# Optimization experiments

Measured on AMD Instinct MI355X. Metric: run time of the kernel, lower is better.

## Reference

```python
import jax, jax.numpy as jnp
import numpy as np

B, T, N = 32, 2048, 2048
D, L, TE, H = 512, 256, 1024, 8

def _ln(x, g, b, eps=1e-5):
    m = x.mean(-1, keepdims=True)
    v = ((x - m) ** 2).mean(-1, keepdims=True)
    return (x - m) / jnp.sqrt(v + eps) * g + b

def setup_inputs() -> dict:
    key = jax.random.key(0)
    ks = jax.random.split(key, 12)
    s = 0.02
    return {
        "x": jax.random.normal(ks[0], (B, T, D), jnp.float32),
        "xf": jax.random.normal(ks[1], (B, N, L), jnp.float32),
        "emb": jax.random.normal(ks[2], (B, TE), jnp.float32),
        "norm_g": jnp.ones((D,), jnp.float32),
        "norm_b": jnp.zeros((D,), jnp.float32),
        "tnorm_g": jnp.ones((L,), jnp.float32),
        "tnorm_b": jnp.zeros((L,), jnp.float32),
        "Wq": jax.random.normal(ks[3], (D, D), jnp.float32) * s,
        "bq": jnp.zeros((D,), jnp.float32),
        "Wk": jax.random.normal(ks[4], (L, D), jnp.float32) * s,
        "bk": jnp.zeros((D,), jnp.float32),
        "Wv": jax.random.normal(ks[5], (L, D), jnp.float32) * s,
        "bv": jnp.zeros((D,), jnp.float32),
        "We": jax.random.normal(ks[6], (TE, 2 * D), jnp.float32) * s,
        "be": jnp.zeros((2 * D,), jnp.float32),
        "snorm_g": jnp.ones((D,), jnp.float32),
        "snorm_b": jnp.zeros((D,), jnp.float32),
        "Wo": jax.random.normal(ks[7], (D, D), jnp.float32) * s,
        "bo": jnp.zeros((D,), jnp.float32),
    }

def reference(x, xf, emb, norm_g, norm_b, tnorm_g, tnorm_b, Wq, bq, Wk, bk, Wv, bv,
              We, be, snorm_g, snorm_b, Wo, bo):
    b, t, d = x.shape
    n = xf.shape[1]
    hd = d // H
    # projections with pre-LayerNorms
    q = (_ln(x, norm_g, norm_b) @ Wq + bq).reshape(b, t, H, hd)
    xfn = _ln(xf, tnorm_g, tnorm_b)
    k = (xfn @ Wk + bk).reshape(b, n, H, hd)
    v = (xfn @ Wv + bv).reshape(b, n, H, hd)
    # dual softmax of linear attention: query over head-dim, key over sequence
    q = jax.nn.softmax(q, axis=-1)
    k = jax.nn.softmax(k, axis=1)
    # O(N*d^2) linear attention
    attn = jnp.einsum('bnhd,bnhl->bhdl', k, v)          # [B,H,hd,hd]
    y = jnp.einsum('bthd,bhdl->bthl', q, attn).reshape(b, t, d)
    # StylizationBlock (dropout is identity in eval)
    emb_out = jax.nn.silu(emb) @ We + be                # [B, 2D]
    scale, shift = emb_out[:, None, :d], emb_out[:, None, d:]
    h = _ln(y, snorm_g, snorm_b) * (1.0 + scale) + shift
    h = jax.nn.silu(h) @ Wo + bo
    return x + h
```

## Files before the change

### kernel.cpp

```cpp
#include <hip/hip_runtime.h>
#include <math.h>

#define B_ 32
#define T_ 2048
#define N_ 2048
#define D_ 512
#define L_ 256
#define TE_ 1024
#define H_ 8
#define MROWS 65536
#define KCH 16

typedef __attribute__((ext_vector_type(8))) short short8;
typedef __attribute__((ext_vector_type(4))) float f32x4;

__device__ __forceinline__ unsigned short f2bf(float f) {
  unsigned u = __float_as_uint(f);
  unsigned r = (u + 0x7FFF + ((u >> 16) & 1)) >> 16;
  return (unsigned short)r;
}
__device__ __forceinline__ float bf2f(unsigned short u) {
  return __uint_as_float(((unsigned)u) << 16);
}
__device__ __forceinline__ void gload_lds16(const void* g, void* l) {
  __builtin_amdgcn_global_load_lds(
      (const __attribute__((address_space(1))) void*)g,
      (__attribute__((address_space(3))) void*)l, 16, 0, 0);
}

__device__ __forceinline__ float blockReduceSum(float v, float* ws) {
#pragma unroll
  for (int m = 32; m >= 1; m >>= 1) v += __shfl_xor(v, m, 64);
  int wid = threadIdx.x >> 6;
  int lane = threadIdx.x & 63;
  __syncthreads();
  if (lane == 0) ws[wid] = v;
  __syncthreads();
  return ws[0] + ws[1] + ws[2] + ws[3];
}

template <int COLS>
__global__ void __launch_bounds__(256) ln_rows(const float* __restrict__ in,
                                               const float* __restrict__ g,
                                               const float* __restrict__ bb,
                                               unsigned short* __restrict__ out) {
  constexpr int E = COLS / 256;
  __shared__ float ws[4];
  size_t row = blockIdx.x;
  const float* rp = in + row * COLS;
  float v[E];
  float s = 0.f;
#pragma unroll
  for (int e = 0; e < E; ++e) {
    v[e] = rp[threadIdx.x + e * 256];
    s += v[e];
  }
  s = blockReduceSum(s, ws);
  float mean = s * (1.0f / COLS);
  float q = 0.f;
#pragma unroll
  for (int e = 0; e < E; ++e) {
    float d = v[e] - mean;
    q += d * d;
  }
  q = blockReduceSum(q, ws);
  float rstd = rsqrtf(q * (1.0f / COLS) + 1e-5f);
  unsigned short* op = out + row * COLS;
#pragma unroll
  for (int e = 0; e < E; ++e) {
    int c = threadIdx.x + e * 256;
    op[c] = f2bf((v[e] - mean) * rstd * g[c] + bb[c]);
  }
}

__global__ void __launch_bounds__(256) transcast(const float* __restrict__ W,
                                                 unsigned short* __restrict__ Wt,
                                                 int K, int Ncols) {
  __shared__ float t[32][33];
  int k0 = blockIdx.x * 32, n0 = blockIdx.y * 32;
  int tx = threadIdx.x & 31, ty = threadIdx.x >> 5;
#pragma unroll
  for (int i = 0; i < 32; i += 8)
    t[ty + i][tx] = W[(size_t)(k0 + ty + i) * Ncols + n0 + tx];
  __syncthreads();
#pragma unroll
  for (int i = 0; i < 32; i += 8)
    Wt[(size_t)(n0 + ty + i) * K + k0 + tx] = f2bf(t[tx][ty + i]);
}

template <int KT, bool ADD, bool OUTBF>
__global__ void __launch_bounds__(256) gemm_mfma(const unsigned short* __restrict__ A,
                                                 const unsigned short* __restrict__ Wt,
                                                 const float* __restrict__ bias,
                                                 const float* __restrict__ add,
                                                 void* __restrict__ Cv) {
  __shared__ __align__(16) unsigned short sA[128 * 32];
  __shared__ __align__(16) unsigned short sB[128 * 32];
  int tid = threadIdx.x;
  int w = tid >> 6, lane = tid & 63;
  int quad = lane >> 4, r16 = lane & 15;
  int wr = w >> 1, wc = w & 1;
  size_t m0 = (size_t)blockIdx.y * 128;
  int n0 = blockIdx.x * 128;
  int srow = lane >> 2;
  int scol = (lane & 3) * 8;
  f32x4 acc[4][4] = {};

  for (int k0 = 0; k0 < KT; k0 += 32) {
    __syncthreads();
#pragma unroll
    for (int i = 0; i < 2; ++i) {
      int seg = w * 2 + i;
      gload_lds16(&A[(m0 + seg * 16 + srow) * KT + k0 + scol], &sA[seg * 512]);
    }
#pragma unroll
    for (int i = 0; i < 2; ++i) {
      int seg = w * 2 + i;
      gload_lds16(&Wt[(size_t)(n0 + seg * 16 + srow) * KT + k0 + scol], &sB[seg * 512]);
    }
    __syncthreads();
    short8 af[4], bfr[4];
#pragma unroll
    for (int mi = 0; mi < 4; ++mi)
      af[mi] = *(const short8*)&sA[(wr * 64 + mi * 16 + r16) * 32 + quad * 8];
#pragma unroll
    for (int ni = 0; ni < 4; ++ni)
      bfr[ni] = *(const short8*)&sB[(wc * 64 + ni * 16 + r16) * 32 + quad * 8];
#pragma unroll
    for (int mi = 0; mi < 4; ++mi)
#pragma unroll
      for (int ni = 0; ni < 4; ++ni)
        acc[mi][ni] = __builtin_amdgcn_mfma_f32_16x16x32_bf16(af[mi], bfr[ni], acc[mi][ni], 0, 0, 0);
  }

  float* Cf = (float*)Cv;
  unsigned short* Cb = (unsigned short*)Cv;
#pragma unroll
  for (int mi = 0; mi < 4; ++mi)
#pragma unroll
    for (int r = 0; r < 4; ++r) {
      size_t grow = m0 + wr * 64 + mi * 16 + quad * 4 + r;
#pragma unroll
      for (int ni = 0; ni < 4; ++ni) {
        int gcol = n0 + wc * 64 + ni * 16 + r16;
        float val = acc[mi][ni][r] + bias[gcol];
        if constexpr (ADD) val += add[grow * 512 + gcol];
        if constexpr (OUTBF)
          Cb[grow * 512 + gcol] = f2bf(val);
        else
          Cf[grow * 512 + gcol] = val;
      }
    }
}

__global__ void __launch_bounds__(256) qsoftmax(unsigned short* __restrict__ q) {
  size_t w = (size_t)blockIdx.x * 4 + (threadIdx.x >> 6);
  int lane = threadIdx.x & 63;
  size_t idx = w * 64 + lane;
  float v = bf2f(q[idx]);
  float m = v;
#pragma unroll
  for (int s = 32; s >= 1; s >>= 1) m = fmaxf(m, __shfl_xor(m, s, 64));
  float e = expf(v - m);
  float ssum = e;
#pragma unroll
  for (int s = 32; s >= 1; s >>= 1) ssum += __shfl_xor(ssum, s, 64);
  q[idx] = f2bf(e / ssum);
}

__global__ void __launch_bounds__(256) kstats_part(const float* __restrict__ k,
                                                   float* __restrict__ pmax,
                                                   float* __restrict__ psum) {
  int b = blockIdx.x, cg = blockIdx.y, ch = blockIdx.z;
  int tid = threadIdx.x;
  int lane = tid & 63, slice = tid >> 6;
  int c = cg * 64 + lane;
  constexpr int ROWS = N_ / KCH;
  constexpr int PT = ROWS / 4;
  const float* kp = k + ((size_t)b * N_ + (size_t)ch * ROWS) * D_ + c;
  float v[PT];
#pragma unroll
  for (int i = 0; i < PT; ++i) v[i] = kp[(size_t)(slice + i * 4) * D_];
  float m = v[0];
#pragma unroll
  for (int i = 1; i < PT; ++i) m = fmaxf(m, v[i]);
  float s = 0.f;
#pragma unroll
  for (int i = 0; i < PT; ++i) s += expf(v[i] - m);
  __shared__ float mred[256], sred[256];
  mred[tid] = m;
  sred[tid] = s;
  __syncthreads();
  if (tid < 64) {
    float m0 = mred[tid], m1 = mred[tid + 64], m2 = mred[tid + 128], m3 = mred[tid + 192];
    float mm = fmaxf(fmaxf(m0, m1), fmaxf(m2, m3));
    float ss = sred[tid] * expf(m0 - mm) + sred[tid + 64] * expf(m1 - mm) +
               sred[tid + 128] * expf(m2 - mm) + sred[tid + 192] * expf(m3 - mm);
    pmax[((size_t)b * KCH + ch) * D_ + cg * 64 + tid] = mm;
    psum[((size_t)b * KCH + ch) * D_ + cg * 64 + tid] = ss;
  }
}

__global__ void __launch_bounds__(256) kstats_comb(const float* __restrict__ pmax,
                                                   const float* __restrict__ psum,
                                                   float* __restrict__ kmax,
                                                   float* __restrict__ ksum) {
  int b = blockIdx.x;
  int c = blockIdx.y * 256 + threadIdx.x;
  float pm[KCH];
#pragma unroll
  for (int ch = 0; ch < KCH; ++ch) pm[ch] = pmax[((size_t)b * KCH + ch) * D_ + c];
  float m = pm[0];
#pragma unroll
  for (int ch = 1; ch < KCH; ++ch) m = fmaxf(m, pm[ch]);
  float s = 0.f;
#pragma unroll
  for (int ch = 0; ch < KCH; ++ch)
    s += psum[((size_t)b * KCH + ch) * D_ + c] * expf(pm[ch] - m);
  kmax[b * D_ + c] = m;
  ksum[b * D_ + c] = s;
}

__global__ void __launch_bounds__(256) attn_kernel(const float* __restrict__ k,
                                                   const float* __restrict__ v,
                                                   const float* __restrict__ kmax,
                                                   const float* __restrict__ ksum,
                                                   float* __restrict__ attn) {
  int b = blockIdx.x, h = blockIdx.y, nc = blockIdx.z;
  int tid = threadIdx.x;
  __shared__ float ks_[32][68];
  __shared__ float vs_[32][68];
  __shared__ float mx[64], is_[64];
  if (tid < 64) {
    mx[tid] = kmax[b * D_ + h * 64 + tid];
    is_[tid] = 1.f / ksum[b * D_ + h * 64 + tid];
  }
  const float* kp = k + ((size_t)b * N_ + nc * 256) * D_ + h * 64;
  const float* vp = v + ((size_t)b * N_ + nc * 256) * D_ + h * 64;
  float acc[4][4] = {};
  int tx = tid & 15, ty = tid >> 4;
  int lr = tid >> 4;
  int c4 = (tid & 15) * 4;
  for (int n0 = 0; n0 < 256; n0 += 32) {
    __syncthreads();
#pragma unroll
    for (int rr = 0; rr < 32; rr += 16) {
      float4 kv = *(const float4*)&kp[(size_t)(n0 + lr + rr) * D_ + c4];
      float4 vv = *(const float4*)&vp[(size_t)(n0 + lr + rr) * D_ + c4];
      ks_[lr + rr][c4 + 0] = expf(kv.x - mx[c4 + 0]) * is_[c4 + 0];
      ks_[lr + rr][c4 + 1] = expf(kv.y - mx[c4 + 1]) * is_[c4 + 1];
      ks_[lr + rr][c4 + 2] = expf(kv.z - mx[c4 + 2]) * is_[c4 + 2];
      ks_[lr + rr][c4 + 3] = expf(kv.w - mx[c4 + 3]) * is_[c4 + 3];
      vs_[lr + rr][c4 + 0] = vv.x;
      vs_[lr + rr][c4 + 1] = vv.y;
      vs_[lr + rr][c4 + 2] = vv.z;
      vs_[lr + rr][c4 + 3] = vv.w;
    }
    __syncthreads();
#pragma unroll
    for (int nn = 0; nn < 32; ++nn) {
      float av[4], bv2[4];
#pragma unroll
      for (int i = 0; i < 4; ++i) av[i] = ks_[nn][ty * 4 + i];
#pragma unroll
      for (int j = 0; j < 4; ++j) bv2[j] = vs_[nn][tx * 4 + j];
#pragma unroll
      for (int i = 0; i < 4; ++i)
#pragma unroll
        for (int j = 0; j < 4; ++j) acc[i][j] += av[i] * bv2[j];
    }
  }
  float* ap = attn + (size_t)(b * H_ + h) * 4096;
#pragma unroll
  for (int i = 0; i < 4; ++i)
#pragma unroll
    for (int j = 0; j < 4; ++j)
      atomicAdd(&ap[(ty * 4 + i) * 64 + tx * 4 + j], acc[i][j]);
}

__global__ void __launch_bounds__(256) embmod(const float* __restrict__ emb,
                                              const float* __restrict__ We,
                                              const float* __restrict__ be,
                                              float* __restrict__ eo) {
  int b = blockIdx.x, tid = threadIdx.x;
  __shared__ float se[TE_];
  for (int i = tid; i < TE_; i += 256) {
    float e = emb[b * TE_ + i];
    se[i] = e / (1.f + expf(-e));
  }
  __syncthreads();
  int j0 = tid * 4;
  float a0 = 0, a1 = 0, a2 = 0, a3 = 0;
  for (int i = 0; i < TE_; ++i) {
    float s = se[i];
    float4 wv = *(const float4*)&We[(size_t)i * 1024 + j0];
    a0 += s * wv.x;
    a1 += s * wv.y;
    a2 += s * wv.z;
    a3 += s * wv.w;
  }
  eo[b * 1024 + j0 + 0] = a0 + be[j0 + 0];
  eo[b * 1024 + j0 + 1] = a1 + be[j0 + 1];
  eo[b * 1024 + j0 + 2] = a2 + be[j0 + 2];
  eo[b * 1024 + j0 + 3] = a3 + be[j0 + 3];
}

__global__ void __launch_bounds__(256) yein(const unsigned short* __restrict__ q,
                                            const float* __restrict__ attn,
                                            float* __restrict__ y) {
  int t0 = blockIdx.x * 32, h = blockIdx.y, b = blockIdx.z;
  int tid = threadIdx.x;
  __shared__ float at[64][68];
  __shared__ float qs[32][68];
  const float* ap = attn + (size_t)(b * H_ + h) * 4096;
  for (int i = tid; i < 4096; i += 256) at[i >> 6][i & 63] = ap[i];
  const unsigned short* qp = q + ((size_t)b * T_ + t0) * D_ + h * 64;
  for (int i = tid; i < 2048; i += 256)
    qs[i >> 6][i & 63] = bf2f(qp[(size_t)(i >> 6) * D_ + (i & 63)]);
  __syncthreads();
  int r = tid >> 3, c0 = (tid & 7) * 8;
  float acc[8] = {};
#pragma unroll
  for (int d = 0; d < 64; ++d) {
    float qv = qs[r][d];
#pragma unroll
    for (int j = 0; j < 8; ++j) acc[j] += qv * at[d][c0 + j];
  }
  float* yp = y + ((size_t)b * T_ + t0 + r) * D_ + h * 64 + c0;
#pragma unroll
  for (int j = 0; j < 8; ++j) yp[j] = acc[j];
}

__global__ void __launch_bounds__(256) modln(const float* __restrict__ y,
                                             const float* __restrict__ sg,
                                             const float* __restrict__ sb,
                                             const float* __restrict__ eo,
                                             unsigned short* __restrict__ hs) {
  __shared__ float ws[4];
  size_t row = blockIdx.x;
  int b = (int)(row >> 11);
  const float* rp = y + row * D_;
  float v[2];
  float s = 0.f;
#pragma unroll
  for (int e = 0; e < 2; ++e) {
    v[e] = rp[threadIdx.x + e * 256];
    s += v[e];
  }
  s = blockReduceSum(s, ws);
  float mean = s * (1.0f / D_);
  float q = 0.f;
#pragma unroll
  for (int e = 0; e < 2; ++e) {
    float d = v[e] - mean;
    q += d * d;
  }
  q = blockReduceSum(q, ws);
  float rstd = rsqrtf(q * (1.0f / D_) + 1e-5f);
#pragma unroll
  for (int e = 0; e < 2; ++e) {
    int c = threadIdx.x + e * 256;
    float xm = (v[e] - mean) * rstd * sg[c] + sb[c];
    float sc = eo[b * 1024 + c];
    float sh = eo[b * 1024 + D_ + c];
    float hm = xm * (1.f + sc) + sh;
    hs[row * D_ + c] = f2bf(hm / (1.f + expf(-hm)));
  }
}

extern "C" void kernel_launch(void* const* d_in, const int* in_sizes, int n_in,
                              void* d_out, int out_size, void* d_ws, size_t ws_size,
                              hipStream_t stream) {
  const float* x = (const float*)d_in[0];
  const float* xf = (const float*)d_in[1];
  const float* emb = (const float*)d_in[2];
  const float* norm_g = (const float*)d_in[3];
  const float* norm_b = (const float*)d_in[4];
  const float* tnorm_g = (const float*)d_in[5];
  const float* tnorm_b = (const float*)d_in[6];
  const float* Wq = (const float*)d_in[7];
  const float* bq = (const float*)d_in[8];
  const float* Wk = (const float*)d_in[9];
  const float* bk = (const float*)d_in[10];
  const float* Wv = (const float*)d_in[11];
  const float* bv = (const float*)d_in[12];
  const float* We = (const float*)d_in[13];
  const float* be = (const float*)d_in[14];
  const float* sg = (const float*)d_in[15];
  const float* sb = (const float*)d_in[16];
  const float* Wo = (const float*)d_in[17];
  const float* bo = (const float*)d_in[18];
  float* out = (float*)d_out;

  float* w = (float*)d_ws;
  unsigned short* qbf = (unsigned short*)w;
  float* kbuf = w + 16777216;
  float* vbuf = w + 16777216 + 33554432;
  unsigned short* xnbf = (unsigned short*)(w + 83886080);
  unsigned short* xfnbf = (unsigned short*)(w + 100663296);
  float* attn = w + 109051904;
  float* kmaxp = attn + 1048576;
  float* ksump = kmaxp + 16384;
  float* embout = ksump + 16384;
  unsigned short* wqt = (unsigned short*)(embout + 32768);
  unsigned short* wkt = wqt + 262144;
  unsigned short* wvt = wkt + 131072;
  unsigned short* wot = wvt + 131072;
  float* pmaxp = w + 83886080;
  float* psump = pmaxp + (size_t)B_ * KCH * D_;

  transcast<<<dim3(16, 16), 256, 0, stream>>>(Wq, wqt, 512, 512);
  transcast<<<dim3(8, 16), 256, 0, stream>>>(Wk, wkt, 256, 512);
  transcast<<<dim3(8, 16), 256, 0, stream>>>(Wv, wvt, 256, 512);
  transcast<<<dim3(16, 16), 256, 0, stream>>>(Wo, wot, 512, 512);
  ln_rows<512><<<MROWS, 256, 0, stream>>>(x, norm_g, norm_b, xnbf);
  gemm_mfma<512, false, true><<<dim3(4, 512), 256, 0, stream>>>(xnbf, wqt, bq, nullptr, qbf);
  ln_rows<256><<<MROWS, 256, 0, stream>>>(xf, tnorm_g, tnorm_b, xfnbf);
  gemm_mfma<256, false, false><<<dim3(4, 512), 256, 0, stream>>>(xfnbf, wkt, bk, nullptr, kbuf);
  gemm_mfma<256, false, false><<<dim3(4, 512), 256, 0, stream>>>(xfnbf, wvt, bv, nullptr, vbuf);
  kstats_part<<<dim3(32, 8, KCH), 256, 0, stream>>>(kbuf, pmaxp, psump);
  kstats_comb<<<dim3(32, 2), 256, 0, stream>>>(pmaxp, psump, kmaxp, ksump);
  hipMemsetAsync(attn, 0, (size_t)1048576 * 4, stream);
  attn_kernel<<<dim3(32, 8, 8), 256, 0, stream>>>(kbuf, vbuf, kmaxp, ksump, attn);
  embmod<<<32, 256, 0, stream>>>(emb, We, be, embout);
  qsoftmax<<<131072, 256, 0, stream>>>(qbf);
  yein<<<dim3(64, 8, 32), 256, 0, stream>>>(qbf, attn, kbuf);
  modln<<<MROWS, 256, 0, stream>>>(kbuf, sg, sb, embout, xnbf);
  gemm_mfma<512, true, false><<<dim3(4, 512), 256, 0, stream>>>(xnbf, wot, bo, x, out);
}
```

Before: 1.076 ms.

## Fuse query softmax into yein and replace attn atomics with partial-sum reduction

The separate qsoftmax pass over the bf16 query buffer is removed. The head-dim softmax is now computed inside yein on the tile already staged in shared memory, and normalization is applied to the output as a 1/sum scale. The atomicAdd accumulation of the per-chunk K^T V products, along with its memset, is replaced by plain float4 stores of per-chunk partials and a small reduce kernel. This removes a full read-modify-write pass over q and the atomic contention, at the cost of an extra launch and extra syncthreads in yein.

```diff
diff --git a/kernel.cpp b/kernel.cpp
--- a/kernel.cpp
+++ b/kernel.cpp
@@ -10,6 +10,7 @@
 #define H_ 8
 #define MROWS 65536
 #define KCH 16
+#define NC_ 8
 
 typedef __attribute__((ext_vector_type(8))) short short8;
 typedef __attribute__((ext_vector_type(4))) float f32x4;
@@ -153,21 +154,6 @@
     }
 }
 
-__global__ void __launch_bounds__(256) qsoftmax(unsigned short* __restrict__ q) {
-  size_t w = (size_t)blockIdx.x * 4 + (threadIdx.x >> 6);
-  int lane = threadIdx.x & 63;
-  size_t idx = w * 64 + lane;
-  float v = bf2f(q[idx]);
-  float m = v;
-#pragma unroll
-  for (int s = 32; s >= 1; s >>= 1) m = fmaxf(m, __shfl_xor(m, s, 64));
-  float e = expf(v - m);
-  float ssum = e;
-#pragma unroll
-  for (int s = 32; s >= 1; s >>= 1) ssum += __shfl_xor(ssum, s, 64);
-  q[idx] = f2bf(e / ssum);
-}
-
 __global__ void __launch_bounds__(256) kstats_part(const float* __restrict__ k,
                                                    float* __restrict__ pmax,
                                                    float* __restrict__ psum) {
@@ -221,11 +207,11 @@
   ksum[b * D_ + c] = s;
 }
 
-__global__ void __launch_bounds__(256) attn_kernel(const float* __restrict__ k,
-                                                   const float* __restrict__ v,
-                                                   const float* __restrict__ kmax,
-                                                   const float* __restrict__ ksum,
-                                                   float* __restrict__ attn) {
+__global__ void __launch_bounds__(256) attn_part_kernel(const float* __restrict__ k,
+                                                        const float* __restrict__ v,
+                                                        const float* __restrict__ kmax,
+                                                        const float* __restrict__ ksum,
+                                                        float* __restrict__ part) {
   int b = blockIdx.x, h = blockIdx.y, nc = blockIdx.z;
   int tid = threadIdx.x;
   __shared__ float ks_[32][68];
@@ -270,12 +256,29 @@
         for (int j = 0; j < 4; ++j) acc[i][j] += av[i] * bv2[j];
     }
   }
-  float* ap = attn + (size_t)(b * H_ + h) * 4096;
-#pragma unroll
-  for (int i = 0; i < 4; ++i)
-#pragma unroll
-    for (int j = 0; j < 4; ++j)
-      atomicAdd(&ap[(ty * 4 + i) * 64 + tx * 4 + j], acc[i][j]);
+  float* ap = part + ((size_t)(b * H_ + h) * NC_ + nc) * 4096;
+#pragma unroll
+  for (int i = 0; i < 4; ++i) {
+    float4 st = make_float4(acc[i][0], acc[i][1], acc[i][2], acc[i][3]);
+    *(float4*)&ap[(ty * 4 + i) * 64 + tx * 4] = st;
+  }
+}
+
+__global__ void __launch_bounds__(256) attn_reduce(const float* __restrict__ part,
+                                                   float* __restrict__ attn) {
+  size_t o = ((size_t)blockIdx.x * 256 + threadIdx.x) * 4;
+  size_t bh = o >> 12;
+  size_t e = o & 4095;
+  float4 s = make_float4(0.f, 0.f, 0.f, 0.f);
+#pragma unroll
+  for (int nc = 0; nc < NC_; ++nc) {
+    float4 p = *(const float4*)&part[(bh * NC_ + nc) * 4096 + e];
+    s.x += p.x;
+    s.y += p.y;
+    s.z += p.z;
+    s.w += p.w;
+  }
+  *(float4*)&attn[o] = s;
 }
 
 __global__ void __launch_bounds__(256) embmod(const float* __restrict__ emb,
@@ -319,6 +322,26 @@
     qs[i >> 6][i & 63] = bf2f(qp[(size_t)(i >> 6) * D_ + (i & 63)]);
   __syncthreads();
   int r = tid >> 3, c0 = (tid & 7) * 8;
+  float lv[8];
+#pragma unroll
+  for (int j = 0; j < 8; ++j) lv[j] = qs[r][c0 + j];
+  float m = lv[0];
+#pragma unroll
+  for (int j = 1; j < 8; ++j) m = fmaxf(m, lv[j]);
+#pragma unroll
+  for (int s = 4; s >= 1; s >>= 1) m = fmaxf(m, __shfl_xor(m, s, 64));
+  float ssum = 0.f;
+#pragma unroll
+  for (int j = 0; j < 8; ++j) {
+    lv[j] = expf(lv[j] - m);
+    ssum += lv[j];
+  }
+#pragma unroll
+  for (int s = 4; s >= 1; s >>= 1) ssum += __shfl_xor(ssum, s, 64);
+  float inv = 1.f / ssum;
+#pragma unroll
+  for (int j = 0; j < 8; ++j) qs[r][c0 + j] = lv[j];
+  __syncthreads();
   float acc[8] = {};
 #pragma unroll
   for (int d = 0; d < 64; ++d) {
@@ -328,7 +351,7 @@
   }
   float* yp = y + ((size_t)b * T_ + t0 + r) * D_ + h * 64 + c0;
 #pragma unroll
-  for (int j = 0; j < 8; ++j) yp[j] = acc[j];
+  for (int j = 0; j < 8; ++j) yp[j] = acc[j] * inv;
 }
 
 __global__ void __launch_bounds__(256) modln(const float* __restrict__ y,
@@ -408,6 +431,7 @@
   unsigned short* wot = wvt + 131072;
   float* pmaxp = w + 83886080;
   float* psump = pmaxp + (size_t)B_ * KCH * D_;
+  float* attnpart = w + 100663296;
 
   transcast<<<dim3(16, 16), 256, 0, stream>>>(Wq, wqt, 512, 512);
   transcast<<<dim3(8, 16), 256, 0, stream>>>(Wk, wkt, 256, 512);
@@ -420,10 +444,9 @@
   gemm_mfma<256, false, false><<<dim3(4, 512), 256, 0, stream>>>(xfnbf, wvt, bv, nullptr, vbuf);
   kstats_part<<<dim3(32, 8, KCH), 256, 0, stream>>>(kbuf, pmaxp, psump);
   kstats_comb<<<dim3(32, 2), 256, 0, stream>>>(pmaxp, psump, kmaxp, ksump);
-  hipMemsetAsync(attn, 0, (size_t)1048576 * 4, stream);
-  attn_kernel<<<dim3(32, 8, 8), 256, 0, stream>>>(kbuf, vbuf, kmaxp, ksump, attn);
+  attn_part_kernel<<<dim3(32, 8, NC_), 256, 0, stream>>>(kbuf, vbuf, kmaxp, ksump, attnpart);
+  attn_reduce<<<1024, 256, 0, stream>>>(attnpart, attn);
   embmod<<<32, 256, 0, stream>>>(emb, We, be, embout);
-  qsoftmax<<<131072, 256, 0, stream>>>(qbf);
   yein<<<dim3(64, 8, 32), 256, 0, stream>>>(qbf, attn, kbuf);
   modln<<<MROWS, 256, 0, stream>>>(kbuf, sg, sb, embout, xnbf);
   gemm_mfma<512, true, false><<<dim3(4, 512), 256, 0, stream>>>(xnbf, wot, bo, x, out);
```

Result: faster. 946.0 us (-12.1%).
